# Optimization experiments

Hardware: AMD Instinct MI355X
Metric: run time of the kernel (lower is better)

Reference implementation:

```python
import jax, jax.numpy as jnp
import numpy as np

N = 4096
IN_DIM = 512
OUT_DIM = 64
NUM_HEADS = 8
DENSITY = 0.01  # adjacency density


def setup_inputs() -> dict:
    key = jax.random.key(0)
    ks = jax.random.split(key, 9)
    h = jax.random.normal(ks[0], (N, IN_DIM), dtype=jnp.float32)
    # sparse adjacency realized as a dense 0/1 mask (the module calls A.to_dense())
    A = (jax.random.uniform(ks[1], (N, N)) < DENSITY).astype(jnp.float32)
    s_in = 1.0 / np.sqrt(IN_DIM)
    Wq = jax.random.normal(ks[2], (IN_DIM, OUT_DIM * NUM_HEADS), dtype=jnp.float32) * s_in
    bq = jax.random.normal(ks[3], (OUT_DIM * NUM_HEADS,), dtype=jnp.float32) * s_in
    Wk = jax.random.normal(ks[4], (IN_DIM, OUT_DIM * NUM_HEADS), dtype=jnp.float32) * s_in
    bk = jax.random.normal(ks[5], (OUT_DIM * NUM_HEADS,), dtype=jnp.float32) * s_in
    Wv = jax.random.normal(ks[6], (IN_DIM, OUT_DIM * NUM_HEADS), dtype=jnp.float32) * s_in
    bv = jax.random.normal(ks[7], (OUT_DIM * NUM_HEADS,), dtype=jnp.float32) * s_in
    return {"A": A, "h": h, "Wq": Wq, "bq": bq, "Wk": Wk, "bk": bk, "Wv": Wv, "bv": bv}


def reference(A, h, Wq, bq, Wk, bk, Wv, bv):
    n = h.shape[0]
    scaling = OUT_DIM ** (-0.5)
    # (N, out_dim, H) to match torch .reshape(N, out_dim, num_heads)
    q = ((h @ Wq) + bq).reshape(n, OUT_DIM, NUM_HEADS) * scaling
    k = ((h @ Wk) + bk).reshape(n, OUT_DIM, NUM_HEADS)
    v = ((h @ Wv) + bv).reshape(n, OUT_DIM, NUM_HEADS)
    # attn[h,n,m] = sum_d q[n,d,h] * k[m,d,h], masked by dense adjacency
    attn = jnp.einsum('ndh,mdh->hnm', q, k) * A[None, :, :]
    # NOTE: original code softmaxes over dim=0 == the HEAD axis (faithful)
    attn = jax.nn.softmax(attn, axis=0)
    # out[h,n,d] = sum_m attn[h,n,m] * v[m,d,h]
    out = jnp.einsum('hnm,mdh->hnd', attn, v)
    # raw row-major reshape of (H, N, D) -> (N, H*D), as in the original
    return out.reshape(n, -1)
```

## Files before the change

kernel.cpp:

```cpp
#include <hip/hip_runtime.h>

typedef unsigned short u16;
typedef unsigned short u16x8 __attribute__((ext_vector_type(8)));
typedef __bf16 bf16x8 __attribute__((ext_vector_type(8)));
typedef float f32x4 __attribute__((ext_vector_type(4)));

#define NN 4096
#define KD 512
#define HD 512
#define CAP 96

__device__ __forceinline__ u16 f2bf(float f) {
    unsigned u = __builtin_bit_cast(unsigned, f);
    u += 0x7fffu + ((u >> 16) & 1u);
    return (u16)(u >> 16);
}
__device__ __forceinline__ float bf2f(u16 u) {
    return __builtin_bit_cast(float, ((unsigned)u) << 16);
}
__device__ __forceinline__ int permj(int j) { return ((j & 7) << 6) | (j >> 3); }

#define GLOAD16(gp, lp) \
    __builtin_amdgcn_global_load_lds((const __attribute__((address_space(1))) void*)(gp), \
                                     (__attribute__((address_space(3))) void*)(lp), 16, 0, 0)

__global__ __launch_bounds__(256) void k_prep(const float4* __restrict__ h4,
        u16* __restrict__ hb,
        const float* __restrict__ Wq, const float* __restrict__ Wk,
        const float* __restrict__ Wv, const float* __restrict__ bq,
        const float* __restrict__ bk, const float* __restrict__ bv,
        u16* __restrict__ wt, float* __restrict__ pbias, float* __restrict__ colsum)
{
    __shared__ float tile[32][33];
    const int tid = threadIdx.x;
    if (blockIdx.x >= 2816) {
        colsum[tid] = 0.f;
        colsum[tid + 256] = 0.f;
        return;
    }
    if (blockIdx.x < 2048) {
        int i = blockIdx.x * 256 + tid;
        float4 f = h4[i];
        ((ushort4*)hb)[i] = make_ushort4(f2bf(f.x), f2bf(f.y), f2bf(f.z), f2bf(f.w));
        return;
    }
    const int b2 = blockIdx.x - 2048;
    const int jb = b2 & 15, kb = (b2 >> 4) & 15, z = b2 >> 8;
    const float* W = (z == 0) ? Wq : ((z == 1) ? Wk : Wv);
    const float scale = (z == 0) ? 0.125f : 1.0f;
    const int j0 = jb * 32, k0 = kb * 32;
    const int tx = tid & 31, ty = tid >> 5;
    #pragma unroll
    for (int r = 0; r < 32; r += 8)
        tile[ty + r][tx] = W[(size_t)(k0 + ty + r) * HD + j0 + tx];
    __syncthreads();
    #pragma unroll
    for (int r = 0; r < 32; r += 8) {
        int j = j0 + ty + r;
        wt[(size_t)(z * 512 + permj(j)) * KD + k0 + tx] = f2bf(scale * tile[tx][ty + r]);
    }
    if (kb == 0 && ty == 0) {
        int j = j0 + tx;
        float b = (z == 0) ? bq[j] * 0.125f : ((z == 1) ? bk[j] : bv[j]);
        pbias[z * 512 + permj(j)] = b;
    }
}

__global__ __launch_bounds__(256) void k_gemm(const u16* __restrict__ hb,
        const u16* __restrict__ wt, const float* __restrict__ pbias,
        u16* __restrict__ qbuf, u16* __restrict__ kbuf, u16* __restrict__ vbuf,
        float* __restrict__ colsum)
{
    __shared__ u16 As[64 * 64];
    __shared__ u16 Bs[128 * 64];
    const int tid = threadIdx.x;
    const int w = tid >> 6, lane = tid & 63;
    const int wr = w >> 1, wc = w & 1;
    const int l16 = lane & 15, half = lane >> 4;
    const int row0 = blockIdx.x * 64, col0 = blockIdx.y * 128;
    const int la = lane & 7, lb = lane >> 3;
    const int swcol = ((la ^ lb) << 3);

    const u16* gA[2]; const u16* gB[4];
    u16* lA[2]; u16* lB[4];
    #pragma unroll
    for (int s = 0; s < 2; ++s) {
        int i = w * 2 + s;
        gA[s] = hb + (size_t)(row0 + 8 * i + lb) * KD + swcol;
        lA[s] = As + i * 512;
    }
    #pragma unroll
    for (int s = 0; s < 4; ++s) {
        int i = w * 4 + s;
        gB[s] = wt + (size_t)(col0 + 8 * i + lb) * KD + swcol;
        lB[s] = Bs + i * 512;
    }

    f32x4 acc[2][4] = {};

    for (int kk = 0; kk < KD; kk += 64) {
        #pragma unroll
        for (int s = 0; s < 2; ++s) GLOAD16(gA[s] + kk, lA[s]);
        #pragma unroll
        for (int s = 0; s < 4; ++s) GLOAD16(gB[s] + kk, lB[s]);
        __syncthreads();
        #pragma unroll
        for (int kk2 = 0; kk2 < 2; ++kk2) {
            bf16x8 af[2], bf[4];
            #pragma unroll
            for (int mi = 0; mi < 2; ++mi) {
                int row = wr * 32 + mi * 16 + l16;
                int off = row * 128 + (((kk2 << 6) | (half << 4)) ^ ((l16 & 7) << 4));
                af[mi] = *(const bf16x8*)((const char*)As + off);
            }
            #pragma unroll
            for (int ni = 0; ni < 4; ++ni) {
                int row = wc * 64 + ni * 16 + l16;
                int off = row * 128 + (((kk2 << 6) | (half << 4)) ^ ((l16 & 7) << 4));
                bf[ni] = *(const bf16x8*)((const char*)Bs + off);
            }
            #pragma unroll
            for (int mi = 0; mi < 2; ++mi)
                #pragma unroll
                for (int ni = 0; ni < 4; ++ni)
                    acc[mi][ni] = __builtin_amdgcn_mfma_f32_16x16x32_bf16(
                        af[mi], bf[ni], acc[mi][ni], 0, 0, 0);
        }
        __syncthreads();
    }

    const int seg = blockIdx.y >> 2;
    #pragma unroll
    for (int ni = 0; ni < 4; ++ni) {
        int j = col0 + wc * 64 + ni * 16 + l16;
        float bj = pbias[j];
        float csum = 0.f;
        #pragma unroll
        for (int mi = 0; mi < 2; ++mi) {
            #pragma unroll
            for (int r = 0; r < 4; ++r) {
                int m = row0 + wr * 32 + mi * 16 + half * 4 + r;
                float val = acc[mi][ni][r] + bj;
                if (seg == 0)      qbuf[(size_t)m * 512 + j] = f2bf(val);
                else if (seg == 1) kbuf[(size_t)m * 512 + (j - 512)] = f2bf(val);
                else             { vbuf[(size_t)m * 512 + (j - 1024)] = f2bf(val); csum += val; }
            }
        }
        if (seg == 2) {
            csum += __shfl_xor(csum, 16);
            csum += __shfl_xor(csum, 32);
            if (lane < 16) atomicAdd(&colsum[j - 1024], csum);
        }
    }
}

__global__ __launch_bounds__(256) void k_attn(const float4* __restrict__ A4,
        const u16* __restrict__ qbuf, const u16* __restrict__ kbuf,
        const u16* __restrict__ vbuf, const float* __restrict__ colsum,
        float* __restrict__ out)
{
    const int tid = threadIdx.x, w = tid >> 6, lane = tid & 63;
    const int n = blockIdx.x;
    __shared__ u16   s_idx[CAP];
    __shared__ int   s_cnt;
    __shared__ float s_red[4][512];

    if (tid == 0) s_cnt = 0;
    __syncthreads();

    float qf[8];
    {
        u16x8 qv = *(const u16x8*)(qbuf + (size_t)n * 512 + lane * 8);
        #pragma unroll
        for (int j = 0; j < 8; ++j) qf[j] = bf2f(qv[j]);
    }

    {
        const float4* arow = A4 + (size_t)n * 1024;
        #pragma unroll
        for (int ii = 0; ii < 4; ++ii) {
            int i = ii * 256 + tid;
            float4 a = arow[i];
            if (a.x != 0.f || a.y != 0.f || a.z != 0.f || a.w != 0.f) {
                int m0 = i * 4;
                if (a.x != 0.f) { int p = atomicAdd(&s_cnt, 1); if (p < CAP) s_idx[p] = (u16)m0; }
                if (a.y != 0.f) { int p = atomicAdd(&s_cnt, 1); if (p < CAP) s_idx[p] = (u16)(m0 + 1); }
                if (a.z != 0.f) { int p = atomicAdd(&s_cnt, 1); if (p < CAP) s_idx[p] = (u16)(m0 + 2); }
                if (a.w != 0.f) { int p = atomicAdd(&s_cnt, 1); if (p < CAP) s_idx[p] = (u16)(m0 + 3); }
            }
        }
    }
    __syncthreads();
    const int cnt = min(s_cnt, CAP);
    const size_t loff = (size_t)(lane * 8);

    float acc8[8] = {0.f,0.f,0.f,0.f,0.f,0.f,0.f,0.f};
    int e = w;
    while (e + 12 < cnt) {
        const int m0 = s_idx[e], m1 = s_idx[e + 4], m2 = s_idx[e + 8], m3 = s_idx[e + 12];
        u16x8 k0 = *(const u16x8*)(kbuf + (size_t)m0 * 512 + loff);
        u16x8 k1 = *(const u16x8*)(kbuf + (size_t)m1 * 512 + loff);
        u16x8 k2 = *(const u16x8*)(kbuf + (size_t)m2 * 512 + loff);
        u16x8 k3 = *(const u16x8*)(kbuf + (size_t)m3 * 512 + loff);
        u16x8 v0 = *(const u16x8*)(vbuf + (size_t)m0 * 512 + loff);
        u16x8 v1 = *(const u16x8*)(vbuf + (size_t)m1 * 512 + loff);
        u16x8 v2 = *(const u16x8*)(vbuf + (size_t)m2 * 512 + loff);
        u16x8 v3 = *(const u16x8*)(vbuf + (size_t)m3 * 512 + loff);
        float s0 = 0.f, s1 = 0.f, s2 = 0.f, s3 = 0.f;
        #pragma unroll
        for (int j = 0; j < 8; ++j) {
            s0 += qf[j] * bf2f(k0[j]); s1 += qf[j] * bf2f(k1[j]);
            s2 += qf[j] * bf2f(k2[j]); s3 += qf[j] * bf2f(k3[j]);
        }
        s0 += __shfl_xor(s0, 1); s1 += __shfl_xor(s1, 1); s2 += __shfl_xor(s2, 1); s3 += __shfl_xor(s3, 1);
        s0 += __shfl_xor(s0, 2); s1 += __shfl_xor(s1, 2); s2 += __shfl_xor(s2, 2); s3 += __shfl_xor(s3, 2);
        s0 += __shfl_xor(s0, 4); s1 += __shfl_xor(s1, 4); s2 += __shfl_xor(s2, 4); s3 += __shfl_xor(s3, 4);
        float mx0 = fmaxf(s0, __shfl_xor(s0, 8)),  mx1 = fmaxf(s1, __shfl_xor(s1, 8));
        float mx2 = fmaxf(s2, __shfl_xor(s2, 8)),  mx3 = fmaxf(s3, __shfl_xor(s3, 8));
        mx0 = fmaxf(mx0, __shfl_xor(mx0, 16)); mx1 = fmaxf(mx1, __shfl_xor(mx1, 16));
        mx2 = fmaxf(mx2, __shfl_xor(mx2, 16)); mx3 = fmaxf(mx3, __shfl_xor(mx3, 16));
        mx0 = fmaxf(mx0, __shfl_xor(mx0, 32)); mx1 = fmaxf(mx1, __shfl_xor(mx1, 32));
        mx2 = fmaxf(mx2, __shfl_xor(mx2, 32)); mx3 = fmaxf(mx3, __shfl_xor(mx3, 32));
        float e0 = __expf(s0 - mx0), e1 = __expf(s1 - mx1);
        float e2 = __expf(s2 - mx2), e3 = __expf(s3 - mx3);
        float Z0 = e0 + __shfl_xor(e0, 8), Z1 = e1 + __shfl_xor(e1, 8);
        float Z2 = e2 + __shfl_xor(e2, 8), Z3 = e3 + __shfl_xor(e3, 8);
        Z0 += __shfl_xor(Z0, 16); Z1 += __shfl_xor(Z1, 16); Z2 += __shfl_xor(Z2, 16); Z3 += __shfl_xor(Z3, 16);
        Z0 += __shfl_xor(Z0, 32); Z1 += __shfl_xor(Z1, 32); Z2 += __shfl_xor(Z2, 32); Z3 += __shfl_xor(Z3, 32);
        const float c0 = e0 * __builtin_amdgcn_rcpf(Z0) - 0.125f;
        const float c1 = e1 * __builtin_amdgcn_rcpf(Z1) - 0.125f;
        const float c2 = e2 * __builtin_amdgcn_rcpf(Z2) - 0.125f;
        const float c3 = e3 * __builtin_amdgcn_rcpf(Z3) - 0.125f;
        #pragma unroll
        for (int j = 0; j < 8; ++j)
            acc8[j] += c0 * bf2f(v0[j]) + c1 * bf2f(v1[j])
                     + c2 * bf2f(v2[j]) + c3 * bf2f(v3[j]);
        e += 16;
    }
    while (e + 4 < cnt) {
        const int m0 = s_idx[e], m1 = s_idx[e + 4];
        u16x8 k0 = *(const u16x8*)(kbuf + (size_t)m0 * 512 + loff);
        u16x8 k1 = *(const u16x8*)(kbuf + (size_t)m1 * 512 + loff);
        u16x8 v0 = *(const u16x8*)(vbuf + (size_t)m0 * 512 + loff);
        u16x8 v1 = *(const u16x8*)(vbuf + (size_t)m1 * 512 + loff);
        float s0 = 0.f, s1 = 0.f;
        #pragma unroll
        for (int j = 0; j < 8; ++j) { s0 += qf[j] * bf2f(k0[j]); s1 += qf[j] * bf2f(k1[j]); }
        s0 += __shfl_xor(s0, 1); s1 += __shfl_xor(s1, 1);
        s0 += __shfl_xor(s0, 2); s1 += __shfl_xor(s1, 2);
        s0 += __shfl_xor(s0, 4); s1 += __shfl_xor(s1, 4);
        float mx0 = fmaxf(s0, __shfl_xor(s0, 8)), mx1 = fmaxf(s1, __shfl_xor(s1, 8));
        mx0 = fmaxf(mx0, __shfl_xor(mx0, 16)); mx1 = fmaxf(mx1, __shfl_xor(mx1, 16));
        mx0 = fmaxf(mx0, __shfl_xor(mx0, 32)); mx1 = fmaxf(mx1, __shfl_xor(mx1, 32));
        float e0 = __expf(s0 - mx0), e1 = __expf(s1 - mx1);
        float Z0 = e0 + __shfl_xor(e0, 8), Z1 = e1 + __shfl_xor(e1, 8);
        Z0 += __shfl_xor(Z0, 16); Z1 += __shfl_xor(Z1, 16);
        Z0 += __shfl_xor(Z0, 32); Z1 += __shfl_xor(Z1, 32);
        const float c0 = e0 * __builtin_amdgcn_rcpf(Z0) - 0.125f;
        const float c1 = e1 * __builtin_amdgcn_rcpf(Z1) - 0.125f;
        #pragma unroll
        for (int j = 0; j < 8; ++j)
            acc8[j] += c0 * bf2f(v0[j]) + c1 * bf2f(v1[j]);
        e += 8;
    }
    for (; e < cnt; e += 4) {
        const int m0 = s_idx[e];
        u16x8 k0 = *(const u16x8*)(kbuf + (size_t)m0 * 512 + loff);
        u16x8 v0 = *(const u16x8*)(vbuf + (size_t)m0 * 512 + loff);
        float s0 = 0.f;
        #pragma unroll
        for (int j = 0; j < 8; ++j) s0 += qf[j] * bf2f(k0[j]);
        s0 += __shfl_xor(s0, 1);
        s0 += __shfl_xor(s0, 2);
        s0 += __shfl_xor(s0, 4);
        float mx0 = fmaxf(s0, __shfl_xor(s0, 8));
        mx0 = fmaxf(mx0, __shfl_xor(mx0, 16));
        mx0 = fmaxf(mx0, __shfl_xor(mx0, 32));
        float e0 = __expf(s0 - mx0);
        float Z0 = e0 + __shfl_xor(e0, 8);
        Z0 += __shfl_xor(Z0, 16);
        Z0 += __shfl_xor(Z0, 32);
        const float c0 = e0 * __builtin_amdgcn_rcpf(Z0) - 0.125f;
        #pragma unroll
        for (int j = 0; j < 8; ++j) acc8[j] += c0 * bf2f(v0[j]);
    }

    *(f32x4*)&s_red[w][lane * 8]     = *(f32x4*)&acc8[0];
    *(f32x4*)&s_red[w][lane * 8 + 4] = *(f32x4*)&acc8[4];
    __syncthreads();

    #pragma unroll
    for (int pp = 0; pp < 2; ++pp) {
        int i2 = pp * 256 + tid;
        int hh2 = i2 >> 6, d = i2 & 63;
        float val = s_red[0][i2] + s_red[1][i2] + s_red[2][i2] + s_red[3][i2]
                  + 0.125f * colsum[i2];
        out[(size_t)hh2 * (NN * 64) + (size_t)n * 64 + d] = val;
    }
}

extern "C" void kernel_launch(void* const* d_in, const int* in_sizes, int n_in,
                              void* d_out, int out_size, void* d_ws, size_t ws_size,
                              hipStream_t stream)
{
    const float* A  = (const float*)d_in[0];
    const float* h  = (const float*)d_in[1];
    const float* Wq = (const float*)d_in[2];
    const float* bq = (const float*)d_in[3];
    const float* Wk = (const float*)d_in[4];
    const float* bk = (const float*)d_in[5];
    const float* Wv = (const float*)d_in[6];
    const float* bv = (const float*)d_in[7];
    float* out = (float*)d_out;

    char* ws = (char*)d_ws;
    u16*   qbuf   = (u16*)(ws);
    u16*   kbuf   = (u16*)(ws + (4u  << 20));
    u16*   vbuf   = (u16*)(ws + (8u  << 20));
    u16*   hb     = (u16*)(ws + (12u << 20));
    u16*   wt     = (u16*)(ws + (16u << 20));
    float* pbias  = (float*)(ws + (18u << 20));
    float* colsum = (float*)(ws + (18u << 20) + 8192);

    k_prep<<<dim3(2817), dim3(256), 0, stream>>>((const float4*)h, hb,
            Wq, Wk, Wv, bq, bk, bv, wt, pbias, colsum);
    k_gemm<<<dim3(64, 12), dim3(256), 0, stream>>>(hb, wt, pbias, qbuf, kbuf, vbuf, colsum);
    k_attn<<<dim3(4096), dim3(256), 0, stream>>>((const float4*)A, qbuf, kbuf, vbuf, colsum, out);
}
```

Before: 157.8 us.

## Scan adjacency into global edge lists concurrently with QKV GEMM

Extra blocks are added to the GEMM launch. They stream the dense adjacency matrix and build per-row neighbour index lists in global memory using global atomics, so the large A read overlaps with the projection GEMM instead of running inside the attention kernel. The attention kernel now just loads its precomputed count and indices. Colsum and count zeroing moves to a memset. The change also drops the max-subtraction in the head softmax and removes the 4-way unrolled edge loop, which cuts shuffles but gives up some memory-level parallelism and overflow safety.

```diff
diff --git a/kernel.cpp b/kernel.cpp
--- a/kernel.cpp
+++ b/kernel.cpp
@@ -1,6 +1,7 @@
 #include <hip/hip_runtime.h>
 
 typedef unsigned short u16;
+typedef unsigned int u32;
 typedef unsigned short u16x8 __attribute__((ext_vector_type(8)));
 typedef __bf16 bf16x8 __attribute__((ext_vector_type(8)));
 typedef float f32x4 __attribute__((ext_vector_type(4)));
@@ -29,15 +30,10 @@
         const float* __restrict__ Wq, const float* __restrict__ Wk,
         const float* __restrict__ Wv, const float* __restrict__ bq,
         const float* __restrict__ bk, const float* __restrict__ bv,
-        u16* __restrict__ wt, float* __restrict__ pbias, float* __restrict__ colsum)
+        u16* __restrict__ wt, float* __restrict__ pbias)
 {
     __shared__ float tile[32][33];
     const int tid = threadIdx.x;
-    if (blockIdx.x >= 2816) {
-        colsum[tid] = 0.f;
-        colsum[tid + 256] = 0.f;
-        return;
-    }
     if (blockIdx.x < 2048) {
         int i = blockIdx.x * 256 + tid;
         float4 f = h4[i];
@@ -66,18 +62,38 @@
     }
 }
 
-__global__ __launch_bounds__(256) void k_gemm(const u16* __restrict__ hb,
+__global__ __launch_bounds__(256) void k_gemm_edges(const u16* __restrict__ hb,
         const u16* __restrict__ wt, const float* __restrict__ pbias,
         u16* __restrict__ qbuf, u16* __restrict__ kbuf, u16* __restrict__ vbuf,
-        float* __restrict__ colsum)
+        float* __restrict__ colsum,
+        const float4* __restrict__ A4, int* __restrict__ cnt, u16* __restrict__ idx)
 {
     __shared__ u16 As[64 * 64];
     __shared__ u16 Bs[128 * 64];
     const int tid = threadIdx.x;
+
+    if (blockIdx.x >= 768) {
+        const int b2 = blockIdx.x - 768;
+        int t = b2 * 256 + tid;
+        const int stride = 1536 * 256;
+        for (int i = t; i < NN * NN / 4; i += stride) {
+            float4 a = A4[i];
+            if (a.x != 0.f || a.y != 0.f || a.z != 0.f || a.w != 0.f) {
+                int n = i >> 10, m0 = (i & 1023) * 4;
+                if (a.x != 0.f) { int p = atomicAdd(&cnt[n], 1); if (p < CAP) idx[n * CAP + p] = (u16)m0; }
+                if (a.y != 0.f) { int p = atomicAdd(&cnt[n], 1); if (p < CAP) idx[n * CAP + p] = (u16)(m0 + 1); }
+                if (a.z != 0.f) { int p = atomicAdd(&cnt[n], 1); if (p < CAP) idx[n * CAP + p] = (u16)(m0 + 2); }
+                if (a.w != 0.f) { int p = atomicAdd(&cnt[n], 1); if (p < CAP) idx[n * CAP + p] = (u16)(m0 + 3); }
+            }
+        }
+        return;
+    }
+
+    const int bx = blockIdx.x & 63, by = blockIdx.x >> 6;
     const int w = tid >> 6, lane = tid & 63;
     const int wr = w >> 1, wc = w & 1;
     const int l16 = lane & 15, half = lane >> 4;
-    const int row0 = blockIdx.x * 64, col0 = blockIdx.y * 128;
+    const int row0 = bx * 64, col0 = by * 128;
     const int la = lane & 7, lb = lane >> 3;
     const int swcol = ((la ^ lb) << 3);
 
@@ -129,7 +145,7 @@
         __syncthreads();
     }
 
-    const int seg = blockIdx.y >> 2;
+    const int seg = by >> 2;
     #pragma unroll
     for (int ni = 0; ni < 4; ++ni) {
         int j = col0 + wc * 64 + ni * 16 + l16;
@@ -154,19 +170,19 @@
     }
 }
 
-__global__ __launch_bounds__(256) void k_attn(const float4* __restrict__ A4,
-        const u16* __restrict__ qbuf, const u16* __restrict__ kbuf,
-        const u16* __restrict__ vbuf, const float* __restrict__ colsum,
-        float* __restrict__ out)
+__global__ __launch_bounds__(256) void k_attn(const int* __restrict__ cnt_g,
+        const u16* __restrict__ idx_g, const u16* __restrict__ qbuf,
+        const u16* __restrict__ kbuf, const u16* __restrict__ vbuf,
+        const float* __restrict__ colsum, float* __restrict__ out)
 {
     const int tid = threadIdx.x, w = tid >> 6, lane = tid & 63;
     const int n = blockIdx.x;
     __shared__ u16   s_idx[CAP];
-    __shared__ int   s_cnt;
     __shared__ float s_red[4][512];
 
-    if (tid == 0) s_cnt = 0;
-    __syncthreads();
+    const int cnt = min(cnt_g[n], CAP);
+    if (tid < CAP / 2)
+        ((u32*)s_idx)[tid] = ((const u32*)(idx_g + (size_t)n * CAP))[tid];
 
     float qf[8];
     {
@@ -174,69 +190,11 @@
         #pragma unroll
         for (int j = 0; j < 8; ++j) qf[j] = bf2f(qv[j]);
     }
-
-    {
-        const float4* arow = A4 + (size_t)n * 1024;
-        #pragma unroll
-        for (int ii = 0; ii < 4; ++ii) {
-            int i = ii * 256 + tid;
-            float4 a = arow[i];
-            if (a.x != 0.f || a.y != 0.f || a.z != 0.f || a.w != 0.f) {
-                int m0 = i * 4;
-                if (a.x != 0.f) { int p = atomicAdd(&s_cnt, 1); if (p < CAP) s_idx[p] = (u16)m0; }
-                if (a.y != 0.f) { int p = atomicAdd(&s_cnt, 1); if (p < CAP) s_idx[p] = (u16)(m0 + 1); }
-                if (a.z != 0.f) { int p = atomicAdd(&s_cnt, 1); if (p < CAP) s_idx[p] = (u16)(m0 + 2); }
-                if (a.w != 0.f) { int p = atomicAdd(&s_cnt, 1); if (p < CAP) s_idx[p] = (u16)(m0 + 3); }
-            }
-        }
-    }
     __syncthreads();
-    const int cnt = min(s_cnt, CAP);
+
     const size_t loff = (size_t)(lane * 8);
-
     float acc8[8] = {0.f,0.f,0.f,0.f,0.f,0.f,0.f,0.f};
     int e = w;
-    while (e + 12 < cnt) {
-        const int m0 = s_idx[e], m1 = s_idx[e + 4], m2 = s_idx[e + 8], m3 = s_idx[e + 12];
-        u16x8 k0 = *(const u16x8*)(kbuf + (size_t)m0 * 512 + loff);
-        u16x8 k1 = *(const u16x8*)(kbuf + (size_t)m1 * 512 + loff);
-        u16x8 k2 = *(const u16x8*)(kbuf + (size_t)m2 * 512 + loff);
-        u16x8 k3 = *(const u16x8*)(kbuf + (size_t)m3 * 512 + loff);
-        u16x8 v0 = *(const u16x8*)(vbuf + (size_t)m0 * 512 + loff);
-        u16x8 v1 = *(const u16x8*)(vbuf + (size_t)m1 * 512 + loff);
-        u16x8 v2 = *(const u16x8*)(vbuf + (size_t)m2 * 512 + loff);
-        u16x8 v3 = *(const u16x8*)(vbuf + (size_t)m3 * 512 + loff);
-        float s0 = 0.f, s1 = 0.f, s2 = 0.f, s3 = 0.f;
-        #pragma unroll
-        for (int j = 0; j < 8; ++j) {
-            s0 += qf[j] * bf2f(k0[j]); s1 += qf[j] * bf2f(k1[j]);
-            s2 += qf[j] * bf2f(k2[j]); s3 += qf[j] * bf2f(k3[j]);
-        }
-        s0 += __shfl_xor(s0, 1); s1 += __shfl_xor(s1, 1); s2 += __shfl_xor(s2, 1); s3 += __shfl_xor(s3, 1);
-        s0 += __shfl_xor(s0, 2); s1 += __shfl_xor(s1, 2); s2 += __shfl_xor(s2, 2); s3 += __shfl_xor(s3, 2);
-        s0 += __shfl_xor(s0, 4); s1 += __shfl_xor(s1, 4); s2 += __shfl_xor(s2, 4); s3 += __shfl_xor(s3, 4);
-        float mx0 = fmaxf(s0, __shfl_xor(s0, 8)),  mx1 = fmaxf(s1, __shfl_xor(s1, 8));
-        float mx2 = fmaxf(s2, __shfl_xor(s2, 8)),  mx3 = fmaxf(s3, __shfl_xor(s3, 8));
-        mx0 = fmaxf(mx0, __shfl_xor(mx0, 16)); mx1 = fmaxf(mx1, __shfl_xor(mx1, 16));
-        mx2 = fmaxf(mx2, __shfl_xor(mx2, 16)); mx3 = fmaxf(mx3, __shfl_xor(mx3, 16));
-        mx0 = fmaxf(mx0, __shfl_xor(mx0, 32)); mx1 = fmaxf(mx1, __shfl_xor(mx1, 32));
-        mx2 = fmaxf(mx2, __shfl_xor(mx2, 32)); mx3 = fmaxf(mx3, __shfl_xor(mx3, 32));
-        float e0 = __expf(s0 - mx0), e1 = __expf(s1 - mx1);
-        float e2 = __expf(s2 - mx2), e3 = __expf(s3 - mx3);
-        float Z0 = e0 + __shfl_xor(e0, 8), Z1 = e1 + __shfl_xor(e1, 8);
-        float Z2 = e2 + __shfl_xor(e2, 8), Z3 = e3 + __shfl_xor(e3, 8);
-        Z0 += __shfl_xor(Z0, 16); Z1 += __shfl_xor(Z1, 16); Z2 += __shfl_xor(Z2, 16); Z3 += __shfl_xor(Z3, 16);
-        Z0 += __shfl_xor(Z0, 32); Z1 += __shfl_xor(Z1, 32); Z2 += __shfl_xor(Z2, 32); Z3 += __shfl_xor(Z3, 32);
-        const float c0 = e0 * __builtin_amdgcn_rcpf(Z0) - 0.125f;
-        const float c1 = e1 * __builtin_amdgcn_rcpf(Z1) - 0.125f;
-        const float c2 = e2 * __builtin_amdgcn_rcpf(Z2) - 0.125f;
-        const float c3 = e3 * __builtin_amdgcn_rcpf(Z3) - 0.125f;
-        #pragma unroll
-        for (int j = 0; j < 8; ++j)
-            acc8[j] += c0 * bf2f(v0[j]) + c1 * bf2f(v1[j])
-                     + c2 * bf2f(v2[j]) + c3 * bf2f(v3[j]);
-        e += 16;
-    }
     while (e + 4 < cnt) {
         const int m0 = s_idx[e], m1 = s_idx[e + 4];
         u16x8 k0 = *(const u16x8*)(kbuf + (size_t)m0 * 512 + loff);
@@ -249,10 +207,7 @@
         s0 += __shfl_xor(s0, 1); s1 += __shfl_xor(s1, 1);
         s0 += __shfl_xor(s0, 2); s1 += __shfl_xor(s1, 2);
         s0 += __shfl_xor(s0, 4); s1 += __shfl_xor(s1, 4);
-        float mx0 = fmaxf(s0, __shfl_xor(s0, 8)), mx1 = fmaxf(s1, __shfl_xor(s1, 8));
-        mx0 = fmaxf(mx0, __shfl_xor(mx0, 16)); mx1 = fmaxf(mx1, __shfl_xor(mx1, 16));
-        mx0 = fmaxf(mx0, __shfl_xor(mx0, 32)); mx1 = fmaxf(mx1, __shfl_xor(mx1, 32));
-        float e0 = __expf(s0 - mx0), e1 = __expf(s1 - mx1);
+        float e0 = __expf(s0), e1 = __expf(s1);
         float Z0 = e0 + __shfl_xor(e0, 8), Z1 = e1 + __shfl_xor(e1, 8);
         Z0 += __shfl_xor(Z0, 16); Z1 += __shfl_xor(Z1, 16);
         Z0 += __shfl_xor(Z0, 32); Z1 += __shfl_xor(Z1, 32);
@@ -273,10 +228,7 @@
         s0 += __shfl_xor(s0, 1);
         s0 += __shfl_xor(s0, 2);
         s0 += __shfl_xor(s0, 4);
-        float mx0 = fmaxf(s0, __shfl_xor(s0, 8));
-        mx0 = fmaxf(mx0, __shfl_xor(mx0, 16));
-        mx0 = fmaxf(mx0, __shfl_xor(mx0, 32));
-        float e0 = __expf(s0 - mx0);
+        float e0 = __expf(s0);
         float Z0 = e0 + __shfl_xor(e0, 8);
         Z0 += __shfl_xor(Z0, 16);
         Z0 += __shfl_xor(Z0, 32);
@@ -321,9 +273,13 @@
     u16*   wt     = (u16*)(ws + (16u << 20));
     float* pbias  = (float*)(ws + (18u << 20));
     float* colsum = (float*)(ws + (18u << 20) + 8192);
-
-    k_prep<<<dim3(2817), dim3(256), 0, stream>>>((const float4*)h, hb,
-            Wq, Wk, Wv, bq, bk, bv, wt, pbias, colsum);
-    k_gemm<<<dim3(64, 12), dim3(256), 0, stream>>>(hb, wt, pbias, qbuf, kbuf, vbuf, colsum);
-    k_attn<<<dim3(4096), dim3(256), 0, stream>>>((const float4*)A, qbuf, kbuf, vbuf, colsum, out);
-}
+    int*   cnt    = (int*)(ws + (18u << 20) + 8192 + 2048);
+    u16*   idx    = (u16*)(ws + (18u << 20) + 8192 + 2048 + 16384);
+
+    hipMemsetAsync(colsum, 0, 2048 + 16384, stream);
+    k_prep<<<dim3(2816), dim3(256), 0, stream>>>((const float4*)h, hb,
+            Wq, Wk, Wv, bq, bk, bv, wt, pbias);
+    k_gemm_edges<<<dim3(768 + 1536), dim3(256), 0, stream>>>(hb, wt, pbias,
+            qbuf, kbuf, vbuf, colsum, (const float4*)A, cnt, idx);
+    k_attn<<<dim3(4096), dim3(256), 0, stream>>>(cnt, idx, qbuf, kbuf, vbuf, colsum, out);
+}
```

After: 200.0 us. +26.7%, slower.
